# Optimization experiments

Measured on AMD Instinct MI355X. Metric: run time of the kernel, lower is better.

## Reference

```python
import jax, jax.numpy as jnp
import numpy as np


def _hardswish(x):
    return x * jnp.clip(x + 3.0, 0.0, 6.0) / 6.0


def _rel_coords_table(W):
    # [1, 2W-1, 2W-1, 2], log-spaced continuous relative coords (SwinV2)
    rc = jnp.arange(-(W - 1), W, dtype=jnp.float32)
    grid = jnp.stack(jnp.meshgrid(rc, rc, indexing='ij'), axis=-1)[None]
    grid = grid / float(W - 1) * 8.0
    return jnp.sign(grid) * jnp.log2(jnp.abs(grid) + 1.0) / np.float32(np.log2(8.0))


def _rel_pos_index(W):
    # [N, N] int indices into the (2W-1)^2 bias table
    coords = np.stack(np.meshgrid(np.arange(W), np.arange(W), indexing='ij')).reshape(2, -1)
    rel = (coords[:, :, None] - coords[:, None, :]).transpose(1, 2, 0)  # [N, N, 2]
    rel[:, :, 0] += W - 1
    rel[:, :, 1] += W - 1
    rel[:, :, 0] *= 2 * W - 1
    return jnp.asarray(rel.sum(-1))


def setup_inputs() -> dict:
    key = jax.random.key(0)
    ks = jax.random.split(key, 6)
    dim, num_heads, W = 512, 16, 8
    N = W * W
    B, nW = 2048, 64
    return {
        'x': jax.random.normal(ks[0], (B, N, dim), jnp.float32),
        'mask': jax.random.normal(ks[1], (nW, N, N), jnp.float32),
        'w_qkv': jax.random.normal(ks[2], (dim, 3 * dim), jnp.float32) * 0.02,
        'w_out': jax.random.normal(ks[3], (dim, dim), jnp.float32) * 0.02,
        'cpb_w1': jax.random.normal(ks[4], (2, 512), jnp.float32) * 0.02,
        'cpb_w2': jax.random.normal(ks[5], (512, num_heads), jnp.float32) * 0.02,
        'logits_scale': jnp.log(10.0 * jnp.ones((num_heads, 1, 1), jnp.float32)),
        'window_size': W,
        'num_heads': num_heads,
    }


def reference(x, mask, w_qkv, w_out, cpb_w1, cpb_w2, logits_scale, window_size, num_heads):
    B, N, C = x.shape
    hd = C // num_heads
    qkv = (x @ w_qkv).reshape(B, N, 3, num_heads, hd).transpose(2, 0, 3, 1, 4)
    q, k, v = qkv[0], qkv[1], qkv[2]  # [B, H, N, hd]

    # cosine attention (L2-normalized q, k) with clamped learned logit scale
    qn = q / jnp.clip(jnp.linalg.norm(q, axis=-1, keepdims=True), 1e-12)
    kn = k / jnp.clip(jnp.linalg.norm(k, axis=-1, keepdims=True), 1e-12)
    attn = jnp.einsum('bhnd,bhmd->bhnm', qn, kn)
    scale = jnp.exp(jnp.minimum(logits_scale, jnp.log(jnp.float32(100.0))))  # [H,1,1]
    attn = attn * scale[None]

    # continuous position bias via tiny MLP + index gather, sigmoid-scaled
    table = _rel_coords_table(window_size)                       # [1, 2W-1, 2W-1, 2]
    bias_table = (_hardswish(table @ cpb_w1) @ cpb_w2).reshape(-1, num_heads)
    idx = _rel_pos_index(window_size)                            # [N, N]
    bias = bias_table[idx.reshape(-1)].reshape(N, N, num_heads).transpose(2, 0, 1)
    attn = attn + 16.0 * jax.nn.sigmoid(bias)[None]

    if mask is not None:
        nW = mask.shape[0]
        attn = attn.reshape(B // nW, nW, num_heads, N, N) + mask[None, :, None]
        attn = attn.reshape(B, num_heads, N, N)

    # NOTE: original uses nn.Softmax(1) -> softmax over the HEAD axis; replicate faithfully
    attn = jax.nn.softmax(attn, axis=1)

    out = jnp.einsum('bhnm,bhmd->bhnd', attn, v).transpose(0, 2, 1, 3).reshape(B, N, C)
    return out @ w_out
```

## Files before the change

kernel.cpp:

```cpp
#include <hip/hip_runtime.h>
#include <hip/hip_bf16.h>

typedef unsigned short u16;
typedef unsigned int u32;
typedef __attribute__((ext_vector_type(8))) short bf16x8;
typedef __attribute__((ext_vector_type(4))) float f32x4;
typedef __attribute__((ext_vector_type(4))) float float4v;

__device__ __forceinline__ float bf2f(u16 v) {
  union { u32 u; float f; } x; x.u = ((u32)v) << 16; return x.f;
}
__device__ __forceinline__ u16 f2bf(float f) {
  union { u32 u; float f; } x; x.f = f;
  return (u16)((x.u + 0x7fffu + ((x.u >> 16) & 1u)) >> 16);
}

__device__ __forceinline__ void gload16(const void* g, void* l) {
  __builtin_amdgcn_global_load_lds(
      (const __attribute__((address_space(1))) u32*)g,
      (__attribute__((address_space(3))) u32*)l, 16, 0, 0);
}

#define MFMA16(a, bfr, cacc) __builtin_amdgcn_mfma_f32_16x16x32_bf16((a), (bfr), (cacc), 0, 0, 0)


__global__ void convert_bf16_kernel(const float* __restrict__ in,
                                    u16* __restrict__ out, int n8) {
  int t = blockIdx.x * blockDim.x + threadIdx.x;
  if (t >= n8) return;
  const float4v* p = (const float4v*)(in + (size_t)t * 8);
  float4v a = p[0], b = p[1];
  union { bf16x8 v; u16 s[8]; } o;
  o.s[0] = f2bf(a[0]); o.s[1] = f2bf(a[1]); o.s[2] = f2bf(a[2]); o.s[3] = f2bf(a[3]);
  o.s[4] = f2bf(b[0]); o.s[5] = f2bf(b[1]); o.s[6] = f2bf(b[2]); o.s[7] = f2bf(b[3]);
  *(bf16x8*)(out + (size_t)t * 8) = o.v;
}

__global__ void transpose_kernel(const float* __restrict__ in, u16* __restrict__ out,
                                 int R, int C) {
  int t = blockIdx.x * blockDim.x + threadIdx.x;
  if (t >= R * C) return;
  int c = t / R, r = t % R;
  out[t] = f2bf(in[r * C + c]);
}

__global__ void bias_tab_kernel(const float* __restrict__ w1, const float* __restrict__ w2,
                                float* __restrict__ tab) {
  int t = blockIdx.x * blockDim.x + threadIdx.x;
  if (t >= 225 * 16) return;
  int r = t >> 4, h = t & 15;
  int i = r / 15, j = r % 15;
  float gi = (float)(i - 7) * (8.0f / 7.0f);
  float gj = (float)(j - 7) * (8.0f / 7.0f);
  float si = (gi > 0.f) ? 1.f : ((gi < 0.f) ? -1.f : 0.f);
  float sj = (gj > 0.f) ? 1.f : ((gj < 0.f) ? -1.f : 0.f);
  float t0 = si * log2f(fabsf(gi) + 1.0f) * (1.0f / 3.0f);
  float t1 = sj * log2f(fabsf(gj) + 1.0f) * (1.0f / 3.0f);
  float acc = 0.f;
  for (int k = 0; k < 512; ++k) {
    float a = t0 * w1[k] + t1 * w1[512 + k];
    float hs = a * fminf(fmaxf(a + 3.f, 0.f), 6.f) * (1.f / 6.f);
    acc += hs * w2[k * 16 + h];
  }
  tab[t] = acc;
}

__global__ void bias16_kernel(const float* __restrict__ tab, float* __restrict__ b16) {
  int t = blockIdx.x * blockDim.x + threadIdx.x;
  if (t >= 16 * 64 * 64) return;
  int h = t >> 12, nm = t & 4095, n = nm >> 6, m = nm & 63;
  int idx = ((n >> 3) - (m >> 3) + 7) * 15 + ((n & 7) - (m & 7) + 7);
  float b = tab[idx * 16 + h];
  b16[t] = 16.0f / (1.0f + expf(-b));
}

template <bool F32OUT>
__global__ __launch_bounds__(256) void gemm_bt(const u16* __restrict__ A,
                                               const u16* __restrict__ Bt,
                                               void* __restrict__ Cout,
                                               int M, int N, int K) {
  __shared__ u16 lA[128 * 64];
  __shared__ u16 lB[128 * 64];
  const int tid = threadIdx.x;
  const int w = tid >> 6, l = tid & 63;
  const int lg = l >> 4, li = l & 15;
  const int nbn = N >> 7;
  const int nwg = gridDim.x;
  int bidx = blockIdx.x;
  int q = nwg >> 3, r = nwg & 7;
  int xcd = bidx & 7, pos = bidx >> 3;
  int swz = (xcd < r ? xcd * (q + 1) : r * (q + 1) + (xcd - r) * q) + pos;
  int bm = swz / nbn, bn = swz % nbn;
  const int wr = w >> 1, wc = w & 1;

  f32x4 acc[4][4];
#pragma unroll
  for (int i = 0; i < 4; i++)
#pragma unroll
    for (int j = 0; j < 4; j++) acc[i][j] = (f32x4){0.f, 0.f, 0.f, 0.f};

  const u16* Abase = A + (size_t)(bm * 128) * K;
  const u16* Bbase = Bt + (size_t)(bn * 128) * K;

  for (int k0 = 0; k0 < K; k0 += 64) {
#pragma unroll
    for (int i = 0; i < 4; ++i) {
      int c = w * 256 + i * 64 + l;
      int row = c >> 3, kc = c & 7;
      int kcs = kc ^ (row & 7);
      gload16(Abase + (size_t)row * K + k0 + kcs * 8, (u16*)lA + c * 8);
      gload16(Bbase + (size_t)row * K + k0 + kcs * 8, (u16*)lB + c * 8);
    }
    __syncthreads();
#pragma unroll
    for (int kk = 0; kk < 2; ++kk) {
      bf16x8 af[4], bfr[4];
#pragma unroll
      for (int t = 0; t < 4; ++t) {
        int row = wr * 64 + t * 16 + li;
        af[t] = *(const bf16x8*)&lA[row * 64 + (((kk * 4 + lg) ^ (row & 7)) << 3)];
        int col = wc * 64 + t * 16 + li;
        bfr[t] = *(const bf16x8*)&lB[col * 64 + (((kk * 4 + lg) ^ (col & 7)) << 3)];
      }
#pragma unroll
      for (int tm = 0; tm < 4; ++tm)
#pragma unroll
        for (int tn = 0; tn < 4; ++tn)
          acc[tm][tn] = MFMA16(af[tm], bfr[tn], acc[tm][tn]);
    }
    __syncthreads();
  }
  int r0 = bm * 128 + wr * 64 + lg * 4;
  int c0 = bn * 128 + wc * 64 + li;
#pragma unroll
  for (int tm = 0; tm < 4; ++tm)
#pragma unroll
    for (int tn = 0; tn < 4; ++tn)
#pragma unroll
      for (int j = 0; j < 4; ++j) {
        size_t off = (size_t)(r0 + tm * 16 + j) * N + c0 + tn * 16;
        if (F32OUT)
          ((float*)Cout)[off] = acc[tm][tn][j];
        else
          ((u16*)Cout)[off] = f2bf(acc[tm][tn][j]);
      }
}

__device__ __forceinline__ void stage_round(const u16* __restrict__ srcb, int tile,
                                            int r, int tid, u16* dst) {
  int c = r * 512 + tid;
  int row = c >> 3;
  int kcs = (c & 7) ^ (row & 7);
  gload16(srcb + (size_t)row * 512 + tile * 64 + kcs * 8, dst + c * 8);
}

template <int QM, int KS, bool READB>
__device__ __forceinline__ void phase_op(const u16* curA, const u16* curB,
                                         int wm, int wn, int lg, int li,
                                         bf16x8 (&bc)[4], f32x4 (&acc)[8][4]) {
  bf16x8 af[4];
#pragma unroll
  for (int i = 0; i < 4; ++i) {
    int row = wm * 128 + (QM * 4 + i) * 16 + li;
    af[i] = *(const bf16x8*)&curA[row * 64 + (((KS * 4 + lg) ^ (row & 7)) << 3)];
  }
  if (READB) {
#pragma unroll
    for (int nt = 0; nt < 4; ++nt) {
      int col = wn * 64 + nt * 16 + li;
      bc[nt] = *(const bf16x8*)&curB[col * 64 + (((KS * 4 + lg) ^ (col & 7)) << 3)];
    }
  }
  __builtin_amdgcn_s_setprio(1);
#pragma unroll
  for (int i = 0; i < 4; ++i)
#pragma unroll
    for (int nt = 0; nt < 4; ++nt)
      acc[QM * 4 + i][nt] = MFMA16(af[i], bc[nt], acc[QM * 4 + i][nt]);
  __builtin_amdgcn_s_setprio(0);
}

__global__ __launch_bounds__(512, 2) void gemm_qkv256(
    const u16* __restrict__ A, const u16* __restrict__ Bt,
    u16* __restrict__ Cq, const float* __restrict__ lscale) {
  __shared__ u16 lds[69632];
  const int tid = threadIdx.x;
  const int l = tid & 63, w = tid >> 6;
  const int lg = l >> 4, li = l & 15;
  const int wm = w >> 2, wn = w & 3;
  int bidx = blockIdx.x;
  int swz = (bidx & 7) * (gridDim.x >> 3) + (bidx >> 3);
  int bm = swz / 6, bn = swz % 6;
  const u16* Ab = A + (size_t)bm * 256 * 512;
  const u16* Bb = Bt + (size_t)bn * 256 * 512;

  f32x4 acc[8][4];
#pragma unroll
  for (int i = 0; i < 8; ++i)
#pragma unroll
    for (int j = 0; j < 4; ++j) acc[i][j] = (f32x4){0.f, 0.f, 0.f, 0.f};

#pragma unroll
  for (int r = 0; r < 4; ++r) stage_round(Ab, 0, r, tid, lds);
#pragma unroll
  for (int r = 0; r < 4; ++r) stage_round(Bb, 0, r, tid, lds + 32768);
  asm volatile("s_waitcnt vmcnt(0)" ::: "memory");
  __builtin_amdgcn_s_barrier();

#pragma unroll 1
  for (int t = 0; t < 8; ++t) {
    const int s = t & 1;
    u16* curA = lds + s * 16384;
    u16* curB = lds + 32768 + s * 16384;
    u16* nxtA = lds + (s ^ 1) * 16384;
    u16* nxtB = lds + 32768 + (s ^ 1) * 16384;
    if (t < 7) {
#pragma unroll
      for (int r = 0; r < 4; ++r) stage_round(Ab, t + 1, r, tid, nxtA);
#pragma unroll
      for (int r = 0; r < 4; ++r) stage_round(Bb, t + 1, r, tid, nxtB);
    }
    bf16x8 bc[4];
    phase_op<0, 0, true >(curA, curB, wm, wn, lg, li, bc, acc);
    phase_op<1, 0, false>(curA, curB, wm, wn, lg, li, bc, acc);
    phase_op<0, 1, true >(curA, curB, wm, wn, lg, li, bc, acc);
    phase_op<1, 1, false>(curA, curB, wm, wn, lg, li, bc, acc);
    asm volatile("s_waitcnt vmcnt(0)" ::: "memory");
    __builtin_amdgcn_s_barrier();
  }
  __syncthreads();

  const int s_t = bn >> 1;
  const int h0 = (bn & 1) * 8;
  if (s_t < 2) {
#pragma unroll
    for (int g = 0; g < 2; ++g) {
      float sca = 1.0f;
      if (s_t == 0) sca = __expf(fminf(lscale[h0 + wn * 2 + g], 4.6051702f));
#pragma unroll
      for (int mt = 0; mt < 8; ++mt) {
        f32x4 s2;
#pragma unroll
        for (int j = 0; j < 4; ++j)
          s2[j] = acc[mt][2 * g][j] * acc[mt][2 * g][j] +
                  acc[mt][2 * g + 1][j] * acc[mt][2 * g + 1][j];
#pragma unroll
        for (int m = 1; m <= 8; m <<= 1)
#pragma unroll
          for (int j = 0; j < 4; ++j) s2[j] += __shfl_xor(s2[j], m);
#pragma unroll
        for (int j = 0; j < 4; ++j) {
          float rn = sca / fmaxf(sqrtf(s2[j]), 1e-12f);
          acc[mt][2 * g][j] *= rn;
          acc[mt][2 * g + 1][j] *= rn;
        }
      }
    }
  }

  u16* ct = lds;
#pragma unroll
  for (int mt = 0; mt < 8; ++mt)
#pragma unroll
    for (int nt = 0; nt < 4; ++nt)
#pragma unroll
      for (int j = 0; j < 4; ++j)
        ct[(wm * 128 + mt * 16 + lg * 4 + j) * 272 + wn * 64 + nt * 16 + li] =
            f2bf(acc[mt][nt][j]);
  __syncthreads();
#pragma unroll
  for (int r = 0; r < 16; ++r) {
    int id = r * 512 + tid;
    int blk = id >> 8;
    int wi = blk >> 3, ht = blk & 7;
    int off = id & 255;
    int rw = off >> 2, d8 = (off & 3) * 8;
    bf16x8 v = *(const bf16x8*)&ct[(wi * 64 + rw) * 272 + ht * 32 + d8];
    size_t base = ((size_t)(s_t * 16 + h0 + ht) * 2048 + (bm * 4 + wi)) * 2048;
    *(bf16x8*)(Cq + base + rw * 32 + d8) = v;
  }
}

__global__ __launch_bounds__(512, 2) void attn2(const u16* __restrict__ qkv,
                                                const float* __restrict__ mask,
                                                const float* __restrict__ bias16,
                                                u16* __restrict__ aout) {
  __shared__ float S[16 * 16 * 65];
  u16* P16 = (u16*)S;
  float* ob = S;
  const int tid = threadIdx.x;
  const int w = tid >> 6, l = tid & 63;
  const int lg = l >> 4, li = l & 15;
  const int b = blockIdx.x, wm = b & 63;
  const float* mask_w = mask + wm * 4096;

  f32x4 oacc[2][4][2];
#pragma unroll
  for (int hp = 0; hp < 2; ++hp)
#pragma unroll
    for (int i = 0; i < 4; ++i) {
      oacc[hp][i][0] = (f32x4){0.f, 0.f, 0.f, 0.f};
      oacc[hp][i][1] = (f32x4){0.f, 0.f, 0.f, 0.f};
    }

#pragma unroll
  for (int c = 0; c < 4; ++c) {
#pragma unroll
    for (int hp = 0; hp < 2; ++hp) {
      int h = w + hp * 8;
      const u16* qb = qkv + ((size_t)h * 2048 + b) * 2048;
      const u16* kb = qkv + ((size_t)(16 + h) * 2048 + b) * 2048;
      const float* bias_h = bias16 + h * 4096;
      bf16x8 kfc = *(const bf16x8*)(kb + (c * 16 + li) * 32 + lg * 8);
      int mg = c * 16 + li;
#pragma unroll
      for (int tn = 0; tn < 4; ++tn) {
        bf16x8 qt = *(const bf16x8*)(qb + (tn * 16 + li) * 32 + lg * 8);
        f32x4 z = {0.f, 0.f, 0.f, 0.f};
        f32x4 s = MFMA16(qt, kfc, z);
#pragma unroll
        for (int j = 0; j < 4; ++j) {
          int n = tn * 16 + lg * 4 + j;
          S[h * 1040 + li * 65 + n] = s[j] + bias_h[n * 64 + mg] + mask_w[n * 64 + mg];
        }
      }
    }
    __syncthreads();
#pragma unroll
    for (int pp = 0; pp < 2; ++pp) {
      int p = tid + pp * 512;
      int base = (p >> 6) * 65 + (p & 63);
      float mx = -3.0e38f;
#pragma unroll
      for (int hh = 0; hh < 16; ++hh) mx = fmaxf(mx, S[hh * 1040 + base]);
      float sum = 0.f;
#pragma unroll
      for (int hh = 0; hh < 16; ++hh) {
        float e = __expf(S[hh * 1040 + base] - mx);
        S[hh * 1040 + base] = e;
        sum += e;
      }
      float inv = 1.0f / sum;
#pragma unroll
      for (int hh = 0; hh < 16; ++hh)
        P16[(hh * 1040 + base) * 2] = f2bf(S[hh * 1040 + base] * inv);
    }
    __syncthreads();
#pragma unroll
    for (int hp = 0; hp < 2; ++hp) {
      int h = w + hp * 8;
      const u16* vb = qkv + ((size_t)(32 + h) * 2048 + b) * 2048;
      bf16x8 vf[2];
#pragma unroll
      for (int td = 0; td < 2; ++td)
#pragma unroll
        for (int e = 0; e < 8; ++e)
          vf[td][e] = (lg < 2)
                          ? (short)vb[(c * 16 + lg * 8 + e) * 32 + td * 16 + li]
                          : (short)0;
#pragma unroll
      for (int tn = 0; tn < 4; ++tn) {
        bf16x8 pf;
#pragma unroll
        for (int e = 0; e < 8; ++e)
          pf[e] = (lg < 2)
                      ? (short)P16[(h * 1040 + (lg * 8 + e) * 65 + tn * 16 + li) * 2]
                      : (short)0;
        oacc[hp][tn][0] = MFMA16(pf, vf[0], oacc[hp][tn][0]);
        oacc[hp][tn][1] = MFMA16(pf, vf[1], oacc[hp][tn][1]);
      }
    }
    __syncthreads();
  }

#pragma unroll
  for (int tn = 0; tn < 4; ++tn) {
#pragma unroll
    for (int hp = 0; hp < 2; ++hp) {
      int h = w + hp * 8;
#pragma unroll
      for (int td = 0; td < 2; ++td)
#pragma unroll
        for (int j = 0; j < 4; ++j)
          ob[(lg * 4 + j) * 516 + h * 32 + td * 16 + li] = oacc[hp][tn][td][j];
    }
    __syncthreads();
    {
      int rr = tid >> 5, c16 = (tid & 31) * 16;
      const float* src = ob + rr * 516 + c16;
      u16* dst = aout + ((size_t)b * 64 + tn * 16 + rr) * 512 + c16;
#pragma unroll
      for (int half = 0; half < 2; ++half) {
        union { bf16x8 v; u16 u[8]; } o;
#pragma unroll
        for (int e = 0; e < 8; ++e) o.u[e] = f2bf(src[half * 8 + e]);
        *(bf16x8*)(dst + half * 8) = o.v;
      }
    }
    __syncthreads();
  }
}

extern "C" void kernel_launch(void* const* d_in, const int* in_sizes, int n_in,
                              void* d_out, int out_size, void* d_ws, size_t ws_size,
                              hipStream_t stream) {
  const float* x = (const float*)d_in[0];
  const float* mask = (const float*)d_in[1];
  const float* w_qkv = (const float*)d_in[2];
  const float* w_out = (const float*)d_in[3];
  const float* cpb_w1 = (const float*)d_in[4];
  const float* cpb_w2 = (const float*)d_in[5];
  const float* lscale = (const float*)d_in[6];
  float* out = (float*)d_out;

  char* ws = (char*)d_ws;
  u16* wqkvT = (u16*)ws;
  u16* woutT = (u16*)(ws + 1572864ull);
  float* btab = (float*)(ws + 2097152ull);
  float* b16 = (float*)(ws + 2113536ull);
  u16* qkv_ws = (u16*)(ws + 2375680ull);
  u16* xb = (u16*)(ws + 2375680ull + 402653184ull);
  u16* attn_out = xb;

  transpose_kernel<<<(512 * 1536 + 255) / 256, 256, 0, stream>>>(w_qkv, wqkvT, 512, 1536);
  transpose_kernel<<<(512 * 512 + 255) / 256, 256, 0, stream>>>(w_out, woutT, 512, 512);
  bias_tab_kernel<<<(225 * 16 + 255) / 256, 256, 0, stream>>>(cpb_w1, cpb_w2, btab);
  bias16_kernel<<<(16 * 64 * 64 + 255) / 256, 256, 0, stream>>>(btab, b16);

  convert_bf16_kernel<<<(131072 * 64 + 255) / 256, 256, 0, stream>>>(x, xb, 131072 * 64);

  gemm_qkv256<<<3072, 512, 0, stream>>>(xb, wqkvT, qkv_ws, lscale);

  attn2<<<2048, 512, 0, stream>>>(qkv_ws, mask, b16, attn_out);

  gemm_bt<true><<<4096, 256, 0, stream>>>(attn_out, woutT, out, 131072, 512, 512);
}
```

Baseline: 949.1 us.

## Store V transposed from QKV GEMM and restructure GEMM pipeline waits

The QKV GEMM epilogue now writes the V tile transposed (d-major), so the attention kernel can load V fragments with single 16-byte vector loads instead of eight scalar gathers. The GEMM main loop moves its wait and barrier to before the compute, using a partial vmcnt wait so the next tile's loads stay in flight, and the epilogue runs in two halves to fit a smaller LDS buffer. The attention kernel also hoists the Q fragments out of the chunk loop and keeps the softmax values in registers instead of re-reading LDS. The extra epilogue barriers and the register pressure from the hoisted fragments could offset part of the gain.

```diff
diff --git a/kernel.cpp b/kernel.cpp
--- a/kernel.cpp
+++ b/kernel.cpp
@@ -183,7 +183,7 @@
 __global__ __launch_bounds__(512, 2) void gemm_qkv256(
     const u16* __restrict__ A, const u16* __restrict__ Bt,
     u16* __restrict__ Cq, const float* __restrict__ lscale) {
-  __shared__ u16 lds[69632];
+  __shared__ u16 lds[65536];
   const int tid = threadIdx.x;
   const int l = tid & 63, w = tid >> 6;
   const int lg = l >> 4, li = l & 15;
@@ -204,31 +204,33 @@
   for (int r = 0; r < 4; ++r) stage_round(Ab, 0, r, tid, lds);
 #pragma unroll
   for (int r = 0; r < 4; ++r) stage_round(Bb, 0, r, tid, lds + 32768);
-  asm volatile("s_waitcnt vmcnt(0)" ::: "memory");
-  __builtin_amdgcn_s_barrier();
 
 #pragma unroll 1
   for (int t = 0; t < 8; ++t) {
     const int s = t & 1;
     u16* curA = lds + s * 16384;
     u16* curB = lds + 32768 + s * 16384;
-    u16* nxtA = lds + (s ^ 1) * 16384;
-    u16* nxtB = lds + 32768 + (s ^ 1) * 16384;
     if (t < 7) {
+      u16* nxtA = lds + (s ^ 1) * 16384;
+      u16* nxtB = lds + 32768 + (s ^ 1) * 16384;
 #pragma unroll
       for (int r = 0; r < 4; ++r) stage_round(Ab, t + 1, r, tid, nxtA);
 #pragma unroll
       for (int r = 0; r < 4; ++r) stage_round(Bb, t + 1, r, tid, nxtB);
-    }
+      asm volatile("s_waitcnt vmcnt(8)" ::: "memory");
+    } else {
+      asm volatile("s_waitcnt vmcnt(0)" ::: "memory");
+    }
+    __builtin_amdgcn_s_barrier();
+    __builtin_amdgcn_sched_barrier(0);
     bf16x8 bc[4];
     phase_op<0, 0, true >(curA, curB, wm, wn, lg, li, bc, acc);
     phase_op<1, 0, false>(curA, curB, wm, wn, lg, li, bc, acc);
     phase_op<0, 1, true >(curA, curB, wm, wn, lg, li, bc, acc);
     phase_op<1, 1, false>(curA, curB, wm, wn, lg, li, bc, acc);
-    asm volatile("s_waitcnt vmcnt(0)" ::: "memory");
+    __builtin_amdgcn_sched_barrier(0);
     __builtin_amdgcn_s_barrier();
   }
-  __syncthreads();
 
   const int s_t = bn >> 1;
   const int h0 = (bn & 1) * 8;
@@ -256,28 +258,64 @@
         }
       }
     }
-  }
-
-  u16* ct = lds;
-#pragma unroll
-  for (int mt = 0; mt < 8; ++mt)
-#pragma unroll
-    for (int nt = 0; nt < 4; ++nt)
-#pragma unroll
-      for (int j = 0; j < 4; ++j)
-        ct[(wm * 128 + mt * 16 + lg * 4 + j) * 272 + wn * 64 + nt * 16 + li] =
-            f2bf(acc[mt][nt][j]);
-  __syncthreads();
-#pragma unroll
-  for (int r = 0; r < 16; ++r) {
-    int id = r * 512 + tid;
-    int blk = id >> 8;
-    int wi = blk >> 3, ht = blk & 7;
-    int off = id & 255;
-    int rw = off >> 2, d8 = (off & 3) * 8;
-    bf16x8 v = *(const bf16x8*)&ct[(wi * 64 + rw) * 272 + ht * 32 + d8];
-    size_t base = ((size_t)(s_t * 16 + h0 + ht) * 2048 + (bm * 4 + wi)) * 2048;
-    *(bf16x8*)(Cq + base + rw * 32 + d8) = v;
+    u16* ct = lds;
+#pragma unroll
+    for (int p = 0; p < 2; ++p) {
+      if (wm == p) {
+#pragma unroll
+        for (int mt = 0; mt < 8; ++mt)
+#pragma unroll
+          for (int nt = 0; nt < 4; ++nt)
+#pragma unroll
+            for (int j = 0; j < 4; ++j)
+              ct[(mt * 16 + lg * 4 + j) * 272 + wn * 64 + nt * 16 + li] =
+                  f2bf(acc[mt][nt][j]);
+      }
+      __syncthreads();
+#pragma unroll
+      for (int r = 0; r < 8; ++r) {
+        int id = r * 512 + tid;
+        int blk = id >> 8;
+        int wi2 = blk >> 3, ht = blk & 7;
+        int off = id & 255;
+        int rw = off >> 2, d8 = (off & 3) * 8;
+        bf16x8 v = *(const bf16x8*)&ct[(wi2 * 64 + rw) * 272 + ht * 32 + d8];
+        size_t base =
+            ((size_t)(s_t * 16 + h0 + ht) * 2048 + (bm * 4 + p * 2 + wi2)) * 2048;
+        *(bf16x8*)(Cq + base + rw * 32 + d8) = v;
+      }
+      __syncthreads();
+    }
+  } else {
+    u16* ctT = lds;
+#pragma unroll
+    for (int p = 0; p < 2; ++p) {
+      if ((wn >> 1) == p) {
+#pragma unroll
+        for (int mt = 0; mt < 8; ++mt)
+#pragma unroll
+          for (int nt = 0; nt < 4; ++nt)
+#pragma unroll
+            for (int j = 0; j < 4; ++j)
+              ctT[((wn & 1) * 64 + nt * 16 + li) * 264 +
+                  wm * 128 + mt * 16 + lg * 4 + j] = f2bf(acc[mt][nt][j]);
+      }
+      __syncthreads();
+#pragma unroll
+      for (int r = 0; r < 8; ++r) {
+        int id = r * 512 + tid;
+        int colc = id >> 5;
+        int seg = id & 31;
+        bf16x8 v = *(const bf16x8*)&ctT[colc * 264 + seg * 8];
+        int hd = p * 128 + colc;
+        int ht = hd >> 5, d = hd & 31;
+        int row = seg * 8;
+        int wi = row >> 6, n0 = row & 63;
+        size_t base = ((size_t)(32 + h0 + ht) * 2048 + (bm * 4 + wi)) * 2048;
+        *(bf16x8*)(Cq + base + d * 64 + n0) = v;
+      }
+      __syncthreads();
+    }
   }
 }
 
@@ -294,6 +332,15 @@
   const int b = blockIdx.x, wm = b & 63;
   const float* mask_w = mask + wm * 4096;
 
+  bf16x8 qfr[2][4];
+#pragma unroll
+  for (int hp = 0; hp < 2; ++hp) {
+    const u16* qb = qkv + ((size_t)(w + hp * 8) * 2048 + b) * 2048;
+#pragma unroll
+    for (int tn = 0; tn < 4; ++tn)
+      qfr[hp][tn] = *(const bf16x8*)(qb + (tn * 16 + li) * 32 + lg * 8);
+  }
+
   f32x4 oacc[2][4][2];
 #pragma unroll
   for (int hp = 0; hp < 2; ++hp)
@@ -308,16 +355,14 @@
 #pragma unroll
     for (int hp = 0; hp < 2; ++hp) {
       int h = w + hp * 8;
-      const u16* qb = qkv + ((size_t)h * 2048 + b) * 2048;
       const u16* kb = qkv + ((size_t)(16 + h) * 2048 + b) * 2048;
       const float* bias_h = bias16 + h * 4096;
       bf16x8 kfc = *(const bf16x8*)(kb + (c * 16 + li) * 32 + lg * 8);
       int mg = c * 16 + li;
 #pragma unroll
       for (int tn = 0; tn < 4; ++tn) {
-        bf16x8 qt = *(const bf16x8*)(qb + (tn * 16 + li) * 32 + lg * 8);
         f32x4 z = {0.f, 0.f, 0.f, 0.f};
-        f32x4 s = MFMA16(qt, kfc, z);
+        f32x4 s = MFMA16(qfr[hp][tn], kfc, z);
 #pragma unroll
         for (int j = 0; j < 4; ++j) {
           int n = tn * 16 + lg * 4 + j;
@@ -330,34 +375,41 @@
     for (int pp = 0; pp < 2; ++pp) {
       int p = tid + pp * 512;
       int base = (p >> 6) * 65 + (p & 63);
+      float vals[16];
       float mx = -3.0e38f;
 #pragma unroll
-      for (int hh = 0; hh < 16; ++hh) mx = fmaxf(mx, S[hh * 1040 + base]);
+      for (int hh = 0; hh < 16; ++hh) {
+        vals[hh] = S[hh * 1040 + base];
+        mx = fmaxf(mx, vals[hh]);
+      }
       float sum = 0.f;
 #pragma unroll
       for (int hh = 0; hh < 16; ++hh) {
-        float e = __expf(S[hh * 1040 + base] - mx);
-        S[hh * 1040 + base] = e;
+        float e = __expf(vals[hh] - mx);
+        vals[hh] = e;
         sum += e;
       }
       float inv = 1.0f / sum;
 #pragma unroll
       for (int hh = 0; hh < 16; ++hh)
-        P16[(hh * 1040 + base) * 2] = f2bf(S[hh * 1040 + base] * inv);
+        P16[(hh * 1040 + base) * 2] = f2bf(vals[hh] * inv);
     }
     __syncthreads();
 #pragma unroll
     for (int hp = 0; hp < 2; ++hp) {
       int h = w + hp * 8;
-      const u16* vb = qkv + ((size_t)(32 + h) * 2048 + b) * 2048;
+      const u16* vbT = qkv + ((size_t)(32 + h) * 2048 + b) * 2048;
       bf16x8 vf[2];
-#pragma unroll
-      for (int td = 0; td < 2; ++td)
-#pragma unroll
-        for (int e = 0; e < 8; ++e)
-          vf[td][e] = (lg < 2)
-                          ? (short)vb[(c * 16 + lg * 8 + e) * 32 + td * 16 + li]
-                          : (short)0;
+      if (lg < 2) {
+#pragma unroll
+        for (int td = 0; td < 2; ++td)
+          vf[td] = *(const bf16x8*)(vbT + (td * 16 + li) * 64 + c * 16 + lg * 8);
+      } else {
+#pragma unroll
+        for (int td = 0; td < 2; ++td)
+#pragma unroll
+          for (int e = 0; e < 8; ++e) vf[td][e] = 0;
+      }
 #pragma unroll
       for (int tn = 0; tn < 4; ++tn) {
         bf16x8 pf;
```

Result: faster. 921.6 us (-2.9%).
